# Kernel tuning notes

Hardware: AMD Instinct MI355X
Metric: run time of the kernel (lower is better)

## Reference

```python
import jax, jax.numpy as jnp
import numpy as np

IN_DIM, HID, OUT_DIM = 2048, 2560, 2048
KERNEL = 4  # causal depthwise temporal conv width (Griffin uses 4)
C_RGLRU = 8.0  # Griffin's fixed scalar c in a_t = a^(c*r_t)


def setup_inputs() -> dict:
    key = jax.random.key(0)
    ks = jax.random.split(key, 16)
    s = 0.02
    return {
        "x": jax.random.normal(ks[0], (4, 2048, IN_DIM), jnp.float32),
        "Wl": jax.random.normal(ks[1], (IN_DIM, HID), jnp.float32) * s,
        "bl": jnp.zeros((HID,), jnp.float32),
        "Wr": jax.random.normal(ks[2], (IN_DIM, HID), jnp.float32) * s,
        "br": jnp.zeros((HID,), jnp.float32),
        "conv_w": jax.random.normal(ks[3], (KERNEL, 1, HID), jnp.float32) * 0.1,
        "conv_b": jnp.zeros((HID,), jnp.float32),
        "Wa": jax.random.normal(ks[4], (HID, HID), jnp.float32) * s,
        "ba": jnp.zeros((HID,), jnp.float32),
        "Wi": jax.random.normal(ks[5], (HID, HID), jnp.float32) * s,
        "bi": jnp.zeros((HID,), jnp.float32),
        "lam": jax.random.normal(ks[6], (HID,), jnp.float32) + 2.0,  # Lambda; sigmoid(lam)~0.88 decay
        "Wo": jax.random.normal(ks[7], (HID, OUT_DIM), jnp.float32) * s,
        "bo": jnp.zeros((OUT_DIM,), jnp.float32),
    }


def _rg_lru(u, Wa, ba, Wi, bi, lam):
    # u: [B,S,H]. a_t = exp(c * r_t * log sigmoid(lam)); log sigmoid = -softplus(-lam)
    r = jax.nn.sigmoid(jnp.einsum("bsh,hk->bsk", u, Wa) + ba)
    i = jax.nn.sigmoid(jnp.einsum("bsh,hk->bsk", u, Wi) + bi)
    log_a = (-C_RGLRU * jax.nn.softplus(-lam)) * r          # [B,S,H], <= 0
    a = jnp.exp(log_a)
    beta = jnp.sqrt(jnp.maximum(1.0 - jnp.exp(2.0 * log_a), 1e-12))
    drive = beta * (i * u)                                   # [B,S,H]

    def step(h, ab):
        a_t, d_t = ab
        h = a_t * h + d_t
        return h, h

    h0 = jnp.zeros((u.shape[0], u.shape[2]), u.dtype)
    _, hs = jax.lax.scan(step, h0, (a.transpose(1, 0, 2), drive.transpose(1, 0, 2)))
    return hs.transpose(1, 0, 2)  # [B,S,H]


def reference(x, Wl, bl, Wr, br, conv_w, conv_b, Wa, ba, Wi, bi, lam, Wo, bo):
    # left (GLU) branch
    left = jax.nn.gelu(jnp.einsum("bsd,dh->bsh", x, Wl) + bl)
    # right branch: linear -> causal depthwise conv1d -> RG-LRU
    r_in = jnp.einsum("bsd,dh->bsh", x, Wr) + br             # [B,S,H]
    conv = jax.lax.conv_general_dilated(
        r_in, conv_w, window_strides=(1,), padding=[(KERNEL - 1, 0)],
        dimension_numbers=("NWC", "WIO", "NWC"), feature_group_count=HID,
    ) + conv_b
    right = _rg_lru(conv, Wa, ba, Wi, bi, lam)
    return jnp.einsum("bsh,ho->bso", left * right, Wo) + bo
```

## Files before the change

### kernel.cpp

```cpp
#include <hip/hip_runtime.h>
#include <stdint.h>

#define B_ 4
#define S_ 2048
#define D_ 2048
#define H_ 2560
#define O_ 2048
#define M_ (B_*S_)
#define NCH 16
#define LCH (S_/NCH)

typedef __attribute__((ext_vector_type(8))) short bf16x8;
typedef __attribute__((ext_vector_type(4))) float f32x4;

typedef const __attribute__((address_space(1))) unsigned int* gp32;
typedef __attribute__((address_space(3))) unsigned int* lp32;

__device__ __forceinline__ void async_cp16(const unsigned short* g, unsigned short* l) {
    __builtin_amdgcn_global_load_lds((gp32)g, (lp32)l, 16, 0, 0);
}

__device__ __forceinline__ unsigned short f2bf(float f) {
    unsigned int x = __float_as_uint(f);
    x += 0x7fffu + ((x >> 16) & 1u);
    return (unsigned short)(x >> 16);
}
__device__ __forceinline__ float bf2f(unsigned short s) {
    return __uint_as_float(((unsigned int)s) << 16);
}
__device__ __forceinline__ float4 ld_bf4(const unsigned short* p) {
    const uint2 u = *(const uint2*)p;
    float4 r;
    r.x = bf2f((unsigned short)(u.x & 0xffffu));
    r.y = bf2f((unsigned short)(u.x >> 16));
    r.z = bf2f((unsigned short)(u.y & 0xffffu));
    r.w = bf2f((unsigned short)(u.y >> 16));
    return r;
}
__device__ __forceinline__ float fast_sigmoid(float x) { return 1.0f / (1.0f + __expf(-x)); }
__device__ __forceinline__ float gelu_tanh(float x) {
    float t = 0.7978845608028654f * (x + 0.044715f * x * x * x);
    float e = __expf(2.0f * t);
    float th = 1.0f - 2.0f / (e + 1.0f);
    return 0.5f * x * (1.0f + th);
}

__global__ void cast_x_kernel(const float* __restrict__ in, unsigned short* __restrict__ out, int n4) {
    int gid = blockIdx.x * 256 + threadIdx.x;
    if (gid >= n4) return;
    const float4 v = ((const float4*)in)[gid];
    union { unsigned short s[4]; uint2 u; } pk;
    pk.s[0] = f2bf(v.x); pk.s[1] = f2bf(v.y); pk.s[2] = f2bf(v.z); pk.s[3] = f2bf(v.w);
    ((uint2*)out)[gid] = pk.u;
}

__global__ void transpose_cast_kernel(const float* __restrict__ in, unsigned short* __restrict__ out,
                                      int K, int N) {
    __shared__ float tile[64][65];
    const int t = threadIdx.x;
    const int k0 = blockIdx.y * 64, n0 = blockIdx.x * 64;
    const int r = t >> 4, c4 = (t & 15) * 4;
    #pragma unroll
    for (int p = 0; p < 4; ++p) {
        const float4 v = *(const float4*)(in + (size_t)(k0 + p*16 + r) * N + n0 + c4);
        tile[p*16 + r][c4+0] = v.x;
        tile[p*16 + r][c4+1] = v.y;
        tile[p*16 + r][c4+2] = v.z;
        tile[p*16 + r][c4+3] = v.w;
    }
    __syncthreads();
    #pragma unroll
    for (int p = 0; p < 4; ++p) {
        const int nn = n0 + p*16 + r;
        union { unsigned short s[4]; uint2 u; } pk;
        #pragma unroll
        for (int j = 0; j < 4; ++j) pk.s[j] = f2bf(tile[c4 + j][p*16 + r]);
        *(uint2*)(out + (size_t)nn * K + k0 + c4) = pk.u;
    }
}

template <int MODE>
__global__ __launch_bounds__(256, 2) void gemm_kernel(
        const unsigned short* __restrict__ A,
        const unsigned short* __restrict__ Bt,
        const int K,
        const float* __restrict__ bias0,
        const float* __restrict__ bias1,
        void* __restrict__ out0,
        void* __restrict__ out1)
{
    __shared__ __align__(16) unsigned short As[128*32];
    __shared__ __align__(16) unsigned short Bs[128*32];
    const int t = threadIdx.x;
    const int m0 = blockIdx.y * 128;
    const int n0 = blockIdx.x * 128;

    const unsigned short* gA = A  + (size_t)(m0 + (t >> 2)) * K + (t & 3) * 8;
    const unsigned short* gB = Bt + (size_t)(n0 + (t >> 2)) * K + (t & 3) * 8;
    unsigned short* lA0 = As + t * 8;
    unsigned short* lA1 = As + (t + 256) * 8;
    unsigned short* lB0 = Bs + t * 8;
    unsigned short* lB1 = Bs + (t + 256) * 8;
    const size_t gstep = (size_t)64 * K;

    const int lane = t & 63;
    const int w = t >> 6;
    const int wm = (w >> 1) * 64;
    const int wn = (w & 1) * 64;
    const int q8 = (lane >> 4) * 8;
    const int l16 = lane & 15;

    f32x4 acc[4][4];
    #pragma unroll
    for (int i = 0; i < 4; ++i)
        #pragma unroll
        for (int j = 0; j < 4; ++j)
            acc[i][j] = (f32x4){0.f, 0.f, 0.f, 0.f};

    for (int k0 = 0; k0 < K; k0 += 32) {
        async_cp16(gA, lA0);
        async_cp16(gA + gstep, lA1);
        async_cp16(gB, lB0);
        async_cp16(gB + gstep, lB1);
        gA += 32; gB += 32;
        __syncthreads();
        bf16x8 af[4], bfr[4];
        #pragma unroll
        for (int f = 0; f < 4; ++f)
            af[f]  = *(const bf16x8*)(As + (wm + f*16 + l16) * 32 + q8);
        #pragma unroll
        for (int f = 0; f < 4; ++f)
            bfr[f] = *(const bf16x8*)(Bs + (wn + f*16 + l16) * 32 + q8);
        #pragma unroll
        for (int fm = 0; fm < 4; ++fm)
            #pragma unroll
            for (int fn = 0; fn < 4; ++fn)
                acc[fm][fn] = __builtin_amdgcn_mfma_f32_16x16x32_bf16(af[fm], bfr[fn], acc[fm][fn], 0, 0, 0);
        __syncthreads();
    }

    const int rbase = (lane >> 4) * 4;
    #pragma unroll
    for (int fm = 0; fm < 4; ++fm) {
        #pragma unroll
        for (int fn = 0; fn < 4; ++fn) {
            const int cc = n0 + wn + fn * 16 + l16;
            #pragma unroll
            for (int j = 0; j < 4; ++j) {
                const int rr = m0 + wm + fm * 16 + rbase + j;
                float v = acc[fm][fn][j];
                if (MODE == 0) {
                    if (cc < H_) {
                        ((unsigned short*)out0)[(size_t)rr * H_ + cc] = f2bf(gelu_tanh(v + bias0[cc]));
                    } else {
                        const int c2 = cc - H_;
                        ((unsigned short*)out1)[(size_t)rr * H_ + c2] = f2bf(v + bias1[c2]);
                    }
                } else if (MODE == 1) {
                    if (cc < H_) {
                        ((unsigned short*)out0)[(size_t)rr * H_ + cc] = f2bf(fast_sigmoid(v + bias0[cc]));
                    } else {
                        const int c2 = cc - H_;
                        ((unsigned short*)out1)[(size_t)rr * H_ + c2] = f2bf(fast_sigmoid(v + bias1[c2]));
                    }
                } else {
                    ((float*)out0)[(size_t)rr * O_ + cc] = v + bias0[cc];
                }
            }
        }
    }
}

__global__ void conv_kernel(const unsigned short* __restrict__ rin,
                            const float* __restrict__ cw,
                            const float* __restrict__ cb,
                            unsigned short* __restrict__ ub)
{
    const int gid = blockIdx.x * 256 + threadIdx.x;
    const int h = (gid % (H_/4)) * 4;
    const int tmp = gid / (H_/4);
    const int s0 = (tmp % (S_/4)) * 4;
    const int b = tmp / (S_/4);
    const unsigned short* base = rin + (size_t)b * S_ * H_ + h;
    float4 rows[7];
    #pragma unroll
    for (int idx = 0; idx < 7; ++idx) {
        const int s = s0 - 3 + idx;
        if (s >= 0) rows[idx] = ld_bf4(base + (size_t)s * H_);
        else        rows[idx] = make_float4(0.f, 0.f, 0.f, 0.f);
    }
    float4 w[4];
    #pragma unroll
    for (int j = 0; j < 4; ++j) w[j] = *(const float4*)(cw + j * H_ + h);
    const float4 bias = *(const float4*)(cb + h);
    #pragma unroll
    for (int p = 0; p < 4; ++p) {
        float ox = bias.x, oy = bias.y, oz = bias.z, ow = bias.w;
        #pragma unroll
        for (int j = 0; j < 4; ++j) {
            ox += w[j].x * rows[p + j].x;
            oy += w[j].y * rows[p + j].y;
            oz += w[j].z * rows[p + j].z;
            ow += w[j].w * rows[p + j].w;
        }
        const size_t oidx = (size_t)b * S_ * H_ + (size_t)(s0 + p) * H_ + h;
        union { unsigned short s4[4]; uint2 uu; } pk;
        pk.s4[0] = f2bf(ox); pk.s4[1] = f2bf(oy); pk.s4[2] = f2bf(oz); pk.s4[3] = f2bf(ow);
        *(uint2*)(ub + oidx) = pk.uu;
    }
}

__global__ void scan_pass1(const unsigned short* __restrict__ rg,
                           const unsigned short* __restrict__ ig,
                           const unsigned short* __restrict__ ub,
                           const float* __restrict__ lam,
                           float* __restrict__ Asum,
                           float* __restrict__ Hend)
{
    const int tid = blockIdx.x * 256 + threadIdx.x;
    const int h = tid % H_;
    const int t2 = tid / H_;
    const int c = t2 % NCH;
    const int b = t2 / NCH;
    const float kh = -8.0f * log1pf(__expf(-lam[h]));
    size_t idx = ((size_t)b * S_ + (size_t)c * LCH) * H_ + h;
    float A = 1.f, hs = 0.f;
    #pragma unroll 4
    for (int s = 0; s < LCH; ++s, idx += H_) {
        const float rv = bf2f(rg[idx]);
        const float iv = bf2f(ig[idx]);
        const float uv = bf2f(ub[idx]);
        const float a = __expf(kh * rv);
        const float beta = sqrtf(fmaxf(1.f - a * a, 1e-12f));
        hs = a * hs + beta * iv * uv;
        A *= a;
    }
    Asum[tid] = A;
    Hend[tid] = hs;
}

__global__ void scan_pass2(const float* __restrict__ Asum, float* __restrict__ Hend) {
    const int tid = blockIdx.x * 256 + threadIdx.x;
    const int h = tid % H_;
    const int b = tid / H_;
    float hin = 0.f;
    #pragma unroll
    for (int c = 0; c < NCH; ++c) {
        const int q = (b * NCH + c) * H_ + h;
        const float Ac = Asum[q];
        const float he = Hend[q];
        Hend[q] = hin;
        hin = he + Ac * hin;
    }
}

__global__ void scan_pass3(const unsigned short* __restrict__ rg,
                           const unsigned short* __restrict__ ig,
                           const unsigned short* __restrict__ ub,
                           const unsigned short* __restrict__ leftb,
                           const float* __restrict__ lam,
                           const float* __restrict__ Hin,
                           unsigned short* __restrict__ lrb)
{
    const int tid = blockIdx.x * 256 + threadIdx.x;
    const int h = tid % H_;
    const int t2 = tid / H_;
    const int c = t2 % NCH;
    const int b = t2 / NCH;
    const float kh = -8.0f * log1pf(__expf(-lam[h]));
    size_t idx = ((size_t)b * S_ + (size_t)c * LCH) * H_ + h;
    float hs = Hin[tid];
    #pragma unroll 4
    for (int s = 0; s < LCH; ++s, idx += H_) {
        const float rv = bf2f(rg[idx]);
        const float iv = bf2f(ig[idx]);
        const float uv = bf2f(ub[idx]);
        const float lf = bf2f(leftb[idx]);
        const float a = __expf(kh * rv);
        const float beta = sqrtf(fmaxf(1.f - a * a, 1e-12f));
        hs = a * hs + beta * iv * uv;
        lrb[idx] = f2bf(lf * hs);
    }
}

extern "C" void kernel_launch(void* const* d_in, const int* in_sizes, int n_in,
                              void* d_out, int out_size, void* d_ws, size_t ws_size,
                              hipStream_t stream)
{
    const float* x   = (const float*)d_in[0];
    const float* Wl  = (const float*)d_in[1];
    const float* bl  = (const float*)d_in[2];
    const float* Wr  = (const float*)d_in[3];
    const float* br  = (const float*)d_in[4];
    const float* cw  = (const float*)d_in[5];
    const float* cb  = (const float*)d_in[6];
    const float* Wa  = (const float*)d_in[7];
    const float* ba  = (const float*)d_in[8];
    const float* Wi  = (const float*)d_in[9];
    const float* bi  = (const float*)d_in[10];
    const float* lam = (const float*)d_in[11];
    const float* Wo  = (const float*)d_in[12];
    const float* bo  = (const float*)d_in[13];
    float* out = (float*)d_out;
    (void)in_sizes; (void)n_in; (void)out_size;

    const size_t wWlr = (size_t)2 * H_ * D_ * 2;
    const size_t wWai = (size_t)2 * H_ * H_ * 2;
    const size_t wWo  = (size_t)O_ * H_ * 2;
    auto al = [](size_t b) { return (b + 255) & ~(size_t)255; };

    int nchunk = 4;
    for (int n = 1; n <= 4; n *= 2) {
        const size_t Mc = M_ / n;
        const size_t Bc = Mc / S_;
        const size_t need = al(wWlr) + al(wWai) + al(wWo)
                          + 4 * al(Mc * H_ * 2)
                          + 2 * al(Bc * NCH * H_ * 4);
        if (need <= ws_size) { nchunk = n; break; }
    }
    const int Mc = M_ / nchunk;
    const int Bc = Mc / S_;
    const size_t actB = (size_t)Mc * H_ * 2;

    char* p = (char*)d_ws;
    size_t off = 0;
    auto alloc = [&](size_t bytes) -> void* {
        void* q = p + off;
        off += al(bytes);
        return q;
    };
    unsigned short* WlrT  = (unsigned short*)alloc(wWlr);
    unsigned short* WaiT  = (unsigned short*)alloc(wWai);
    unsigned short* WoT   = (unsigned short*)alloc(wWo);
    unsigned short* slotX = (unsigned short*)alloc(actB);
    unsigned short* slotL = (unsigned short*)alloc(actB);
    unsigned short* slotR = (unsigned short*)alloc(actB);
    unsigned short* slotU = (unsigned short*)alloc(actB);
    float* Asum = (float*)alloc((size_t)Bc * NCH * H_ * 4);
    float* Hend = (float*)alloc((size_t)Bc * NCH * H_ * 4);

    transpose_cast_kernel<<<dim3(H_/64, D_/64), dim3(256), 0, stream>>>(Wl, WlrT, D_, H_);
    transpose_cast_kernel<<<dim3(H_/64, D_/64), dim3(256), 0, stream>>>(Wr, WlrT + (size_t)H_*D_, D_, H_);
    transpose_cast_kernel<<<dim3(H_/64, H_/64), dim3(256), 0, stream>>>(Wa, WaiT, H_, H_);
    transpose_cast_kernel<<<dim3(H_/64, H_/64), dim3(256), 0, stream>>>(Wi, WaiT + (size_t)H_*H_, H_, H_);
    transpose_cast_kernel<<<dim3(O_/64, H_/64), dim3(256), 0, stream>>>(Wo, WoT, H_, O_);

    for (int c = 0; c < nchunk; ++c) {
        const float* xc = x + (size_t)c * Mc * D_;
        float* outc = out + (size_t)c * Mc * O_;
        unsigned short* xb    = slotX;
        unsigned short* leftb = slotL;
        unsigned short* rinb  = slotR;
        unsigned short* ub    = slotU;
        unsigned short* rgb   = slotX;
        unsigned short* igb   = slotR;
        unsigned short* lrb   = slotX;

        cast_x_kernel<<<dim3(Mc*D_/4/256), dim3(256), 0, stream>>>(xc, xb, Mc*D_/4);
        gemm_kernel<0><<<dim3((2*H_)/128, Mc/128), dim3(256), 0, stream>>>(xb, WlrT, D_, bl, br, leftb, rinb);
        conv_kernel<<<dim3(Bc*S_*H_/16/256), dim3(256), 0, stream>>>(rinb, cw, cb, ub);
        gemm_kernel<1><<<dim3((2*H_)/128, Mc/128), dim3(256), 0, stream>>>(ub, WaiT, H_, ba, bi, rgb, igb);
        scan_pass1<<<dim3(Bc*NCH*H_/256), dim3(256), 0, stream>>>(rgb, igb, ub, lam, Asum, Hend);
        scan_pass2<<<dim3(Bc*H_/256), dim3(256), 0, stream>>>(Asum, Hend);
        scan_pass3<<<dim3(Bc*NCH*H_/256), dim3(256), 0, stream>>>(rgb, igb, ub, leftb, lam, Hend, lrb);
        gemm_kernel<2><<<dim3(O_/128, Mc/128), dim3(256), 0, stream>>>(lrb, WoT, H_, bo, nullptr, outc, nullptr);
    }
}
```

Measured before the change: 910.7 us.

## Double GEMM K-tile to 64 with XOR-swizzled LDS layout

```diff
diff --git a/kernel.cpp b/kernel.cpp
--- a/kernel.cpp
+++ b/kernel.cpp
@@ -89,25 +89,25 @@
         void* __restrict__ out0,
         void* __restrict__ out1)
 {
-    __shared__ __align__(16) unsigned short As[128*32];
-    __shared__ __align__(16) unsigned short Bs[128*32];
+    __shared__ __align__(16) unsigned short As[128*64];
+    __shared__ __align__(16) unsigned short Bs[128*64];
     const int t = threadIdx.x;
     const int m0 = blockIdx.y * 128;
     const int n0 = blockIdx.x * 128;
 
-    const unsigned short* gA = A  + (size_t)(m0 + (t >> 2)) * K + (t & 3) * 8;
-    const unsigned short* gB = Bt + (size_t)(n0 + (t >> 2)) * K + (t & 3) * 8;
-    unsigned short* lA0 = As + t * 8;
-    unsigned short* lA1 = As + (t + 256) * 8;
-    unsigned short* lB0 = Bs + t * 8;
-    unsigned short* lB1 = Bs + (t + 256) * 8;
-    const size_t gstep = (size_t)64 * K;
+    const int srow = t >> 3;
+    const int csrc = ((t & 7) ^ (srow & 7)) * 8;
+    const unsigned short* gA = A  + (size_t)(m0 + srow) * K + csrc;
+    const unsigned short* gB = Bt + (size_t)(n0 + srow) * K + csrc;
+    unsigned short* lA = As + t * 8;
+    unsigned short* lB = Bs + t * 8;
+    const size_t gstep = (size_t)32 * K;
 
     const int lane = t & 63;
     const int w = t >> 6;
     const int wm = (w >> 1) * 64;
     const int wn = (w & 1) * 64;
-    const int q8 = (lane >> 4) * 8;
+    const int q = lane >> 4;
     const int l16 = lane & 15;
 
     f32x4 acc[4][4];
@@ -117,29 +117,34 @@
         for (int j = 0; j < 4; ++j)
             acc[i][j] = (f32x4){0.f, 0.f, 0.f, 0.f};
 
-    for (int k0 = 0; k0 < K; k0 += 32) {
-        async_cp16(gA, lA0);
-        async_cp16(gA + gstep, lA1);
-        async_cp16(gB, lB0);
-        async_cp16(gB + gstep, lB1);
-        gA += 32; gB += 32;
+    for (int k0 = 0; k0 < K; k0 += 64) {
+        #pragma unroll
+        for (int j = 0; j < 4; ++j) {
+            async_cp16(gA + j * gstep, lA + j * 2048);
+            async_cp16(gB + j * gstep, lB + j * 2048);
+        }
+        gA += 64; gB += 64;
         __syncthreads();
-        bf16x8 af[4], bfr[4];
-        #pragma unroll
-        for (int f = 0; f < 4; ++f)
-            af[f]  = *(const bf16x8*)(As + (wm + f*16 + l16) * 32 + q8);
-        #pragma unroll
-        for (int f = 0; f < 4; ++f)
-            bfr[f] = *(const bf16x8*)(Bs + (wn + f*16 + l16) * 32 + q8);
-        #pragma unroll
-        for (int fm = 0; fm < 4; ++fm)
+        #pragma unroll
+        for (int ks = 0; ks < 2; ++ks) {
+            const int ch = ((q + ks * 4) ^ (l16 & 7)) * 8;
+            bf16x8 af[4], bfr[4];
             #pragma unroll
-            for (int fn = 0; fn < 4; ++fn)
-                acc[fm][fn] = __builtin_amdgcn_mfma_f32_16x16x32_bf16(af[fm], bfr[fn], acc[fm][fn], 0, 0, 0);
+            for (int f = 0; f < 4; ++f)
+                af[f]  = *(const bf16x8*)(As + (wm + f*16 + l16) * 64 + ch);
+            #pragma unroll
+            for (int f = 0; f < 4; ++f)
+                bfr[f] = *(const bf16x8*)(Bs + (wn + f*16 + l16) * 64 + ch);
+            #pragma unroll
+            for (int fm = 0; fm < 4; ++fm)
+                #pragma unroll
+                for (int fn = 0; fn < 4; ++fn)
+                    acc[fm][fn] = __builtin_amdgcn_mfma_f32_16x16x32_bf16(af[fm], bfr[fn], acc[fm][fn], 0, 0, 0);
+        }
         __syncthreads();
     }
 
-    const int rbase = (lane >> 4) * 4;
+    const int rbase = q * 4;
     #pragma unroll
     for (int fm = 0; fm < 4; ++fm) {
         #pragma unroll
```

New measurement: 831.8 us. 1.09x faster.
